# Kernel optimization log

Measured on AMD Instinct MI355X. Metric: run time of the kernel, lower is better.

The kernel has to match this reference:

```python
import jax, jax.numpy as jnp
import numpy as np

N = 10000  # num_users + num_posts


def gcn_conv(x, edge_index, W, b):
    """PyG-style GCNConv: out = D^-1/2 (A+I) D^-1/2 (x W) + b."""
    h = x @ W  # [N, d]
    src, dst = edge_index[0], edge_index[1]
    loop = jnp.arange(N, dtype=src.dtype)
    src = jnp.concatenate([src, loop])
    dst = jnp.concatenate([dst, loop])
    ones = jnp.ones(src.shape[0], dtype=h.dtype)
    deg = jax.ops.segment_sum(ones, dst, num_segments=N)  # in-degree incl. self-loop
    dinv = jnp.where(deg > 0, jax.lax.rsqrt(deg), 0.0)
    norm = dinv[src] * dinv[dst]  # [E+N]
    msg = h[src] * norm[:, None]  # gather + scale
    out = jax.ops.segment_sum(msg, dst, num_segments=N)  # scatter-add
    return out + b


def setup_inputs() -> dict:
    key = jax.random.key(0)
    k1, k2, k3, k4 = jax.random.split(key, 4)
    E = 320000
    H = 64
    x = jax.random.normal(k1, (N, N), dtype=jnp.float32)
    edge_index = jax.random.randint(k2, (2, E), 0, N, dtype=jnp.int64)
    W1 = jax.random.normal(k3, (N, H), dtype=jnp.float32) / np.sqrt(N)
    b1 = jnp.zeros((H,), dtype=jnp.float32)
    W2 = jax.random.normal(k4, (H, H), dtype=jnp.float32) / np.sqrt(H)
    b2 = jnp.zeros((H,), dtype=jnp.float32)
    return {"x": x, "edge_index": edge_index, "W1": W1, "b1": b1, "W2": W2, "b2": b2}


def reference(x, edge_index, W1, b1, W2, b2):
    h = gcn_conv(x, edge_index, W1, b1)
    h = jax.nn.relu(h)
    return gcn_conv(h, edge_index, W2, b2)
```

## Files before the change

kernel.cpp:

```cpp
#include <hip/hip_runtime.h>
#include <hip/hip_bf16.h>

#define NND 10000
#define HD 64
#define KPAD 10112
#define ROWS 64
#define RBLK 157
#define KSTEP 128
#define KHEAD 5632
#define CAP 96
#define ABYTES 32768
#define BBYTES 16384
#define BUFB (ABYTES + BBYTES)
#define GRID 512

typedef __attribute__((ext_vector_type(8))) short bf16x8;
typedef __attribute__((ext_vector_type(4))) float f32x4;

__device__ __forceinline__ short f2bf(float f) {
    unsigned u = __builtin_bit_cast(unsigned, f);
    u += 0x7FFFu + ((u >> 16) & 1u);
    return (short)(u >> 16);
}

__device__ __forceinline__ void gload16(const void* gp, void* lp) {
    __builtin_amdgcn_global_load_lds(
        (const __attribute__((address_space(1))) unsigned int*)gp,
        (__attribute__((address_space(3))) unsigned int*)lp, 16, 0, 0);
}

__device__ __forceinline__ void gload16nt(const void* gp, void* lp) {
    __builtin_amdgcn_global_load_lds(
        (const __attribute__((address_space(1))) unsigned int*)gp,
        (__attribute__((address_space(3))) unsigned int*)lp, 16, 0, 2);
}

__global__ __launch_bounds__(256) void prep2_kernel(const float* __restrict__ W1,
        int* __restrict__ cnt, float* __restrict__ h, short* __restrict__ w1t) {
    __shared__ float tile[64][65];
    const int t = threadIdx.x;
    const int k0 = blockIdx.x * 64;
    #pragma unroll
    for (int i = 0; i < 16; ++i) {
        int r = i * 4 + (t >> 6);
        int c = t & 63;
        int k = k0 + r;
        tile[r][c] = (k < NND) ? W1[(size_t)k * HD + c] : 0.f;
    }
    __syncthreads();
    #pragma unroll
    for (int i = 0; i < 16; ++i) {
        int c = i * 4 + (t >> 6);
        int k = t & 63;
        if (k0 + k < KPAD)
            w1t[(size_t)c * KPAD + k0 + k] = f2bf(tile[k][c]);
    }
    int tid = blockIdx.x * 256 + t;
    if (tid < NND) cnt[tid] = 0;
    f32x4* h4 = (f32x4*)h;
    f32x4 z = {0.f, 0.f, 0.f, 0.f};
    #pragma unroll
    for (int i = 0; i < 4; ++i) {
        int idx = tid + i * 40448;
        if (idx < NND * HD / 4) h4[idx] = z;
    }
}

__global__ __launch_bounds__(512, 1) void csrgemm1_kernel(const float* __restrict__ x,
        const short* __restrict__ w1t, float* __restrict__ h,
        const int* __restrict__ ei, int* __restrict__ cnt, int* __restrict__ csr, int E) {
    {
        const int stride = GRID * 512;
        for (int e = blockIdx.x * 512 + threadIdx.x; e < E; e += stride) {
            int s = ei[e], d = ei[E + e];
            int pos = atomicAdd(&cnt[d], 1);
            if (pos < CAP) csr[d * CAP + pos] = s;
        }
    }
    asm volatile("s_waitcnt vmcnt(0)" ::: "memory");
    __shared__ f32x4 smem4[3 * BUFB / 16];
    char* smem = (char*)smem4;
    const int l = threadIdx.x & 63;
    const int w = threadIdx.x >> 6;
    int g, c, nch;
    {
        const int b = blockIdx.x;
        if (b < 164) { g = b >> 2; c = b & 3; nch = 4; }
        else { int bb = b - 164; int q = bb / 3; g = 41 + q; c = bb - q * 3; nch = 3; }
    }
    const int r0 = g * ROWS;
    int kstart, nsteps;
    if (nch == 4) { kstart = c * 20 * KSTEP; nsteps = (c == 3) ? 19 : 20; }
    else          { kstart = c * 27 * KSTEP; nsteps = (c == 2) ? 25 : 27; }

    const int wr = (w & 3) * 16;
    const int wc = (w >> 2) * 32;
    const int akg = l >> 4;
    const int l15 = l & 15;
    const int l7 = l & 7;

    f32x4 acc[2];
    acc[0] = f32x4{0.f, 0.f, 0.f, 0.f};
    acc[1] = f32x4{0.f, 0.f, 0.f, 0.f};

    union AFU { bf16x8 v; __hip_bfloat162 p[4]; };

    auto stage = [&](int buf, int k0) {
        char* sb = smem + buf * BUFB;
        const bool cached = (k0 < KHEAD);
        #pragma unroll
        for (int i = 0; i < 4; ++i) {
            int row = w * 8 + i * 2 + (l >> 5);
            int rg = r0 + row; if (rg >= NND) rg = 0;
            int pl = ((l & 31) >> 1) ^ (row & 7);
            const char* gp = (const char*)x + (size_t)rg * (NND * 4)
                             + (size_t)k0 * 4 + pl * 32 + (l & 1) * 16;
            if (k0 + pl * 8 + (l & 1) * 4 + 3 >= NND)
                gp = (const char*)x;
            if (cached) gload16(gp, sb + w * 4096 + i * 1024);
            else        gload16nt(gp, sb + w * 4096 + i * 1024);
        }
        #pragma unroll
        for (int j = 0; j < 2; ++j) {
            int col = w * 8 + j * 4 + (l >> 4);
            int cl = (l & 15) ^ (col & 7);
            const char* gp = (const char*)w1t + (size_t)col * (KPAD * 2)
                             + (size_t)k0 * 2 + cl * 16;
            gload16(gp, sb + ABYTES + w * 2048 + j * 1024);
        }
    };

    stage(0, kstart);
    if (nsteps > 1) stage(1, kstart + KSTEP);
    for (int t = 0; t < nsteps; ++t) {
        if (t + 1 < nsteps) asm volatile("s_waitcnt vmcnt(6)" ::: "memory");
        else                asm volatile("s_waitcnt vmcnt(0)" ::: "memory");
        __builtin_amdgcn_s_barrier();
        if (t + 2 < nsteps) stage((t + 2) % 3, kstart + (t + 2) * KSTEP);
        const char* sb = smem + (t % 3) * BUFB;
        #pragma unroll
        for (int ks = 0; ks < 4; ++ks) {
            int cp = (ks * 4 + akg) ^ l7;
            int arow = wr + l15;
            const char* ap = sb + arow * 512 + cp * 32;
            f32x4 a0 = *(const f32x4*)ap;
            f32x4 a1 = *(const f32x4*)(ap + 16);
            AFU af;
            af.p[0] = __float22bfloat162_rn(float2{a0[0], a0[1]});
            af.p[1] = __float22bfloat162_rn(float2{a0[2], a0[3]});
            af.p[2] = __float22bfloat162_rn(float2{a1[0], a1[1]});
            af.p[3] = __float22bfloat162_rn(float2{a1[2], a1[3]});
            #pragma unroll
            for (int cg = 0; cg < 2; ++cg) {
                int col = wc + cg * 16 + l15;
                bf16x8 b = *(const bf16x8*)(sb + ABYTES + col * 256 + cp * 16);
                acc[cg] = __builtin_amdgcn_mfma_f32_16x16x32_bf16(af.v, b, acc[cg], 0, 0, 0);
            }
        }
    }
    {
        const int crow = r0 + wr + akg * 4;
        #pragma unroll
        for (int cg = 0; cg < 2; ++cg) {
            const int ccol = wc + cg * 16 + l15;
            #pragma unroll
            for (int j = 0; j < 4; ++j) {
                int row = crow + j;
                if (row < NND)
                    unsafeAtomicAdd(&h[(size_t)row * HD + ccol], acc[cg][j]);
            }
        }
    }
}

__global__ __launch_bounds__(256) void scale_h_kernel(float* __restrict__ h,
        const int* __restrict__ cnt) {
    const int wave = threadIdx.x >> 6, lane = threadIdx.x & 63;
    const int r = blockIdx.x * 4 + wave;
    if (r >= NND) return;
    const float dd = rsqrtf((float)(min(cnt[r], CAP) + 1));
    h[(size_t)r * HD + lane] *= dd;
}

__global__ __launch_bounds__(256) void agg1g2_kernel(const float* __restrict__ h,
        const int* __restrict__ csr, const int* __restrict__ cnt,
        const float* __restrict__ b1, const float* __restrict__ W2,
        float* __restrict__ h2) {
    __shared__ float w2s[HD * HD];
    __shared__ float rowbuf[4][HD];
    for (int i = threadIdx.x; i < HD * HD; i += 256) w2s[i] = W2[i];
    const int wave = threadIdx.x >> 6, lane = threadIdx.x & 63;
    const int d = blockIdx.x * 4 + wave;
    const int n = min(cnt[d], CAP);
    const float dd = rsqrtf((float)(n + 1));
    float sA = h[(size_t)d * HD + lane];
    float sB = 0.f, sC = 0.f, sD = 0.f;
    float sE = 0.f, sF = 0.f, sG = 0.f, sH = 0.f;
    const int* row = csr + d * CAP;
    int j = 0;
    for (; j + 8 <= n; j += 8) {
        int a0 = row[j],   a1 = row[j+1], a2 = row[j+2], a3 = row[j+3];
        int a4 = row[j+4], a5 = row[j+5], a6 = row[j+6], a7 = row[j+7];
        sA += h[(size_t)a0 * HD + lane];
        sB += h[(size_t)a1 * HD + lane];
        sC += h[(size_t)a2 * HD + lane];
        sD += h[(size_t)a3 * HD + lane];
        sE += h[(size_t)a4 * HD + lane];
        sF += h[(size_t)a5 * HD + lane];
        sG += h[(size_t)a6 * HD + lane];
        sH += h[(size_t)a7 * HD + lane];
    }
    for (; j < n; ++j) sA += h[(size_t)row[j] * HD + lane];
    float sum = ((sA + sB) + (sC + sD)) + ((sE + sF) + (sG + sH));
    float acc = fmaf(sum, dd, b1[lane]);
    rowbuf[wave][lane] = fmaxf(acc, 0.f);
    __syncthreads();
    float s = 0.f;
    #pragma unroll
    for (int k = 0; k < HD; ++k)
        s = fmaf(rowbuf[wave][k], w2s[k * HD + lane], s);
    h2[(size_t)d * HD + lane] = s * dd;
}

__global__ __launch_bounds__(256) void agg2_kernel(const float* __restrict__ feat,
        const int* __restrict__ csr, const int* __restrict__ cnt,
        const float* __restrict__ bias, float* __restrict__ out) {
    const int wave = threadIdx.x >> 6, lane = threadIdx.x & 63;
    const int d = blockIdx.x * 4 + wave;
    const int n = min(cnt[d], CAP);
    const float dd = rsqrtf((float)(n + 1));
    float sA = feat[(size_t)d * HD + lane];
    float sB = 0.f, sC = 0.f, sD = 0.f;
    float sE = 0.f, sF = 0.f, sG = 0.f, sH = 0.f;
    const int* row = csr + d * CAP;
    int j = 0;
    for (; j + 8 <= n; j += 8) {
        int a0 = row[j],   a1 = row[j+1], a2 = row[j+2], a3 = row[j+3];
        int a4 = row[j+4], a5 = row[j+5], a6 = row[j+6], a7 = row[j+7];
        sA += feat[(size_t)a0 * HD + lane];
        sB += feat[(size_t)a1 * HD + lane];
        sC += feat[(size_t)a2 * HD + lane];
        sD += feat[(size_t)a3 * HD + lane];
        sE += feat[(size_t)a4 * HD + lane];
        sF += feat[(size_t)a5 * HD + lane];
        sG += feat[(size_t)a6 * HD + lane];
        sH += feat[(size_t)a7 * HD + lane];
    }
    for (; j < n; ++j) sA += feat[(size_t)row[j] * HD + lane];
    float sum = ((sA + sB) + (sC + sD)) + ((sE + sF) + (sG + sH));
    out[(size_t)d * HD + lane] = fmaf(sum, dd, bias[lane]);
}

extern "C" void kernel_launch(void* const* d_in, const int* in_sizes, int n_in,
                              void* d_out, int out_size, void* d_ws, size_t ws_size,
                              hipStream_t stream) {
    const float* x  = (const float*)d_in[0];
    const int*   ei = (const int*)d_in[1];
    const float* W1 = (const float*)d_in[2];
    const float* b1 = (const float*)d_in[3];
    const float* W2 = (const float*)d_in[4];
    const float* b2 = (const float*)d_in[5];
    float* out = (float*)d_out;
    const int E = in_sizes[1] / 2;

    char* ws = (char*)d_ws;
    int*   cnt  = (int*)(ws);
    float* h    = (float*)(ws + 40000);
    float* h2   = (float*)(ws + 2600000);
    short* w1t  = (short*)(ws + 5160000);
    int*   csr  = (int*)(ws + 6454336);

    prep2_kernel<<<158, 256, 0, stream>>>(W1, cnt, h, w1t);
    csrgemm1_kernel<<<GRID, 512, 0, stream>>>(x, w1t, h, ei, cnt, csr, E);
    scale_h_kernel<<<2500, 256, 0, stream>>>(h, cnt);
    agg1g2_kernel<<<2500, 256, 0, stream>>>(h, csr, cnt, b1, W2, h2);
    agg2_kernel<<<2500, 256, 0, stream>>>(h2, csr, cnt, b2, out);
}
```

Baseline: 130.8 us.

## Fuse scale and two aggregation kernels into one cooperative grid-synced kernel

Replaces three separate launches (scale h, layer-1 aggregation plus W2 matmul, layer-2 aggregation) with a single cooperative kernel of 512 persistent blocks that loop over row quads and separate the phases with grid.sync(). This removes two kernel launch boundaries and their tail drain. In exchange it adds two grid-wide barriers, caps parallelism at 512 blocks of 256 threads with launch bounds asking for 2 blocks per SM, and requires cooperative launch support.

```diff
diff --git a/kernel.cpp b/kernel.cpp
--- a/kernel.cpp
+++ b/kernel.cpp
@@ -1,5 +1,8 @@
 #include <hip/hip_runtime.h>
 #include <hip/hip_bf16.h>
+#include <hip/hip_cooperative_groups.h>
+
+namespace cg = cooperative_groups;
 
 #define NND 10000
 #define HD 64
@@ -173,82 +176,82 @@
     }
 }
 
-__global__ __launch_bounds__(256) void scale_h_kernel(float* __restrict__ h,
-        const int* __restrict__ cnt) {
-    const int wave = threadIdx.x >> 6, lane = threadIdx.x & 63;
-    const int r = blockIdx.x * 4 + wave;
-    if (r >= NND) return;
-    const float dd = rsqrtf((float)(min(cnt[r], CAP) + 1));
-    h[(size_t)r * HD + lane] *= dd;
-}
-
-__global__ __launch_bounds__(256) void agg1g2_kernel(const float* __restrict__ h,
+__global__ __launch_bounds__(256, 2) void fused_agg_kernel(float* __restrict__ h,
         const int* __restrict__ csr, const int* __restrict__ cnt,
         const float* __restrict__ b1, const float* __restrict__ W2,
-        float* __restrict__ h2) {
+        float* __restrict__ h2, const float* __restrict__ b2,
+        float* __restrict__ out) {
+    cg::grid_group grid = cg::this_grid();
     __shared__ float w2s[HD * HD];
     __shared__ float rowbuf[4][HD];
     for (int i = threadIdx.x; i < HD * HD; i += 256) w2s[i] = W2[i];
     const int wave = threadIdx.x >> 6, lane = threadIdx.x & 63;
-    const int d = blockIdx.x * 4 + wave;
-    const int n = min(cnt[d], CAP);
-    const float dd = rsqrtf((float)(n + 1));
-    float sA = h[(size_t)d * HD + lane];
-    float sB = 0.f, sC = 0.f, sD = 0.f;
-    float sE = 0.f, sF = 0.f, sG = 0.f, sH = 0.f;
-    const int* row = csr + d * CAP;
-    int j = 0;
-    for (; j + 8 <= n; j += 8) {
-        int a0 = row[j],   a1 = row[j+1], a2 = row[j+2], a3 = row[j+3];
-        int a4 = row[j+4], a5 = row[j+5], a6 = row[j+6], a7 = row[j+7];
-        sA += h[(size_t)a0 * HD + lane];
-        sB += h[(size_t)a1 * HD + lane];
-        sC += h[(size_t)a2 * HD + lane];
-        sD += h[(size_t)a3 * HD + lane];
-        sE += h[(size_t)a4 * HD + lane];
-        sF += h[(size_t)a5 * HD + lane];
-        sG += h[(size_t)a6 * HD + lane];
-        sH += h[(size_t)a7 * HD + lane];
-    }
-    for (; j < n; ++j) sA += h[(size_t)row[j] * HD + lane];
-    float sum = ((sA + sB) + (sC + sD)) + ((sE + sF) + (sG + sH));
-    float acc = fmaf(sum, dd, b1[lane]);
-    rowbuf[wave][lane] = fmaxf(acc, 0.f);
-    __syncthreads();
-    float s = 0.f;
-    #pragma unroll
-    for (int k = 0; k < HD; ++k)
-        s = fmaf(rowbuf[wave][k], w2s[k * HD + lane], s);
-    h2[(size_t)d * HD + lane] = s * dd;
-}
-
-__global__ __launch_bounds__(256) void agg2_kernel(const float* __restrict__ feat,
-        const int* __restrict__ csr, const int* __restrict__ cnt,
-        const float* __restrict__ bias, float* __restrict__ out) {
-    const int wave = threadIdx.x >> 6, lane = threadIdx.x & 63;
-    const int d = blockIdx.x * 4 + wave;
-    const int n = min(cnt[d], CAP);
-    const float dd = rsqrtf((float)(n + 1));
-    float sA = feat[(size_t)d * HD + lane];
-    float sB = 0.f, sC = 0.f, sD = 0.f;
-    float sE = 0.f, sF = 0.f, sG = 0.f, sH = 0.f;
-    const int* row = csr + d * CAP;
-    int j = 0;
-    for (; j + 8 <= n; j += 8) {
-        int a0 = row[j],   a1 = row[j+1], a2 = row[j+2], a3 = row[j+3];
-        int a4 = row[j+4], a5 = row[j+5], a6 = row[j+6], a7 = row[j+7];
-        sA += feat[(size_t)a0 * HD + lane];
-        sB += feat[(size_t)a1 * HD + lane];
-        sC += feat[(size_t)a2 * HD + lane];
-        sD += feat[(size_t)a3 * HD + lane];
-        sE += feat[(size_t)a4 * HD + lane];
-        sF += feat[(size_t)a5 * HD + lane];
-        sG += feat[(size_t)a6 * HD + lane];
-        sH += feat[(size_t)a7 * HD + lane];
-    }
-    for (; j < n; ++j) sA += feat[(size_t)row[j] * HD + lane];
-    float sum = ((sA + sB) + (sC + sD)) + ((sE + sF) + (sG + sH));
-    out[(size_t)d * HD + lane] = fmaf(sum, dd, bias[lane]);
+    const int nquads = NND / 4;
+    for (int q = blockIdx.x; q < nquads; q += gridDim.x) {
+        int r = q * 4 + wave;
+        const float dd = rsqrtf((float)(min(cnt[r], CAP) + 1));
+        h[(size_t)r * HD + lane] *= dd;
+    }
+    grid.sync();
+    for (int q = blockIdx.x; q < nquads; q += gridDim.x) {
+        const int d = q * 4 + wave;
+        const int n = min(cnt[d], CAP);
+        const float dd = rsqrtf((float)(n + 1));
+        float sA = h[(size_t)d * HD + lane];
+        float sB = 0.f, sC = 0.f, sD = 0.f;
+        float sE = 0.f, sF = 0.f, sG = 0.f, sH = 0.f;
+        const int* row = csr + d * CAP;
+        int j = 0;
+        for (; j + 8 <= n; j += 8) {
+            int a0 = row[j],   a1 = row[j+1], a2 = row[j+2], a3 = row[j+3];
+            int a4 = row[j+4], a5 = row[j+5], a6 = row[j+6], a7 = row[j+7];
+            sA += h[(size_t)a0 * HD + lane];
+            sB += h[(size_t)a1 * HD + lane];
+            sC += h[(size_t)a2 * HD + lane];
+            sD += h[(size_t)a3 * HD + lane];
+            sE += h[(size_t)a4 * HD + lane];
+            sF += h[(size_t)a5 * HD + lane];
+            sG += h[(size_t)a6 * HD + lane];
+            sH += h[(size_t)a7 * HD + lane];
+        }
+        for (; j < n; ++j) sA += h[(size_t)row[j] * HD + lane];
+        float sum = ((sA + sB) + (sC + sD)) + ((sE + sF) + (sG + sH));
+        float acc = fmaf(sum, dd, b1[lane]);
+        rowbuf[wave][lane] = fmaxf(acc, 0.f);
+        __syncthreads();
+        float s = 0.f;
+        #pragma unroll
+        for (int k = 0; k < HD; ++k)
+            s = fmaf(rowbuf[wave][k], w2s[k * HD + lane], s);
+        h2[(size_t)d * HD + lane] = s * dd;
+        __syncthreads();
+    }
+    grid.sync();
+    for (int q = blockIdx.x; q < nquads; q += gridDim.x) {
+        const int d = q * 4 + wave;
+        const int n = min(cnt[d], CAP);
+        const float dd = rsqrtf((float)(n + 1));
+        float sA = h2[(size_t)d * HD + lane];
+        float sB = 0.f, sC = 0.f, sD = 0.f;
+        float sE = 0.f, sF = 0.f, sG = 0.f, sH = 0.f;
+        const int* row = csr + d * CAP;
+        int j = 0;
+        for (; j + 8 <= n; j += 8) {
+            int a0 = row[j],   a1 = row[j+1], a2 = row[j+2], a3 = row[j+3];
+            int a4 = row[j+4], a5 = row[j+5], a6 = row[j+6], a7 = row[j+7];
+            sA += h2[(size_t)a0 * HD + lane];
+            sB += h2[(size_t)a1 * HD + lane];
+            sC += h2[(size_t)a2 * HD + lane];
+            sD += h2[(size_t)a3 * HD + lane];
+            sE += h2[(size_t)a4 * HD + lane];
+            sF += h2[(size_t)a5 * HD + lane];
+            sG += h2[(size_t)a6 * HD + lane];
+            sH += h2[(size_t)a7 * HD + lane];
+        }
+        for (; j < n; ++j) sA += h2[(size_t)row[j] * HD + lane];
+        float sum = ((sA + sB) + (sC + sD)) + ((sE + sF) + (sG + sH));
+        out[(size_t)d * HD + lane] = fmaf(sum, dd, b2[lane]);
+    }
 }
 
 extern "C" void kernel_launch(void* const* d_in, const int* in_sizes, int n_in,
@@ -272,7 +275,8 @@
 
     prep2_kernel<<<158, 256, 0, stream>>>(W1, cnt, h, w1t);
     csrgemm1_kernel<<<GRID, 512, 0, stream>>>(x, w1t, h, ei, cnt, csr, E);
-    scale_h_kernel<<<2500, 256, 0, stream>>>(h, cnt);
-    agg1g2_kernel<<<2500, 256, 0, stream>>>(h, csr, cnt, b1, W2, h2);
-    agg2_kernel<<<2500, 256, 0, stream>>>(h2, csr, cnt, b2, out);
-}
+    void* args[] = {(void*)&h, (void*)&csr, (void*)&cnt, (void*)&b1,
+                    (void*)&W2, (void*)&h2, (void*)&b2, (void*)&out};
+    hipLaunchCooperativeKernel((const void*)fused_agg_kernel, dim3(512), dim3(256),
+                               args, 0, stream);
+}
```

Result: slower. 258.2 us (+97.5%).
